# Performance work log

Hardware: AMD Instinct MI355X
Metric: run time of the kernel (lower is better)

Reference implementation:

```python
import jax, jax.numpy as jnp
import numpy as np

D_STATE = 16
D_CONV = 4
DT_RANK = 8


def layer_norm(x, g, b, eps=1e-5):
    m = x.mean(-1, keepdims=True)
    v = ((x - m) ** 2).mean(-1, keepdims=True)
    return (x - m) / jnp.sqrt(v + eps) * g + b


def rms_norm(x, w, eps=1e-5):
    return x * jax.lax.rsqrt(jnp.mean(x * x, -1, keepdims=True) + eps) * w


def mamba_layer(feat, in_proj_w, conv_w, conv_b, x_proj_w, dt_proj_w, dt_proj_b,
                A_log, D_param, out_proj_w, rms_w):
    # feat: [N, C] treated as a length-N sequence with batch 1 (residual block)
    x_in = rms_norm(feat, rms_w)
    xz = x_in @ in_proj_w                         # [N, 2*d_inner]
    d_inner = conv_w.shape[0]
    x, z = xz[:, :d_inner], xz[:, d_inner:]
    # causal depthwise conv1d (torch pad=d_conv-1 then truncate to L)
    L = x.shape[0]
    x_pad = jnp.pad(x, ((D_CONV - 1, 0), (0, 0)))
    xc = conv_b + sum(x_pad[k:k + L, :] * conv_w[:, k] for k in range(D_CONV))
    x = jax.nn.silu(xc)
    dbc = x @ x_proj_w                            # [N, dt_rank + 2*d_state]
    delta = jax.nn.softplus(dbc[:, :DT_RANK] @ dt_proj_w + dt_proj_b)  # [N, d_inner]
    Bm = dbc[:, DT_RANK:DT_RANK + D_STATE]        # [N, d_state]
    Cm = dbc[:, DT_RANK + D_STATE:]               # [N, d_state]
    A = -jnp.exp(A_log)                           # [d_inner, d_state]

    def step(h, inp):
        d_t, b_t, c_t, x_t = inp
        dA = jnp.exp(d_t[:, None] * A)            # [d_inner, d_state]
        h = dA * h + d_t[:, None] * b_t[None, :] * x_t[:, None]
        y_t = (h * c_t[None, :]).sum(-1)          # [d_inner]
        return h, y_t

    h0 = jnp.zeros((d_inner, D_STATE), feat.dtype)
    _, y = jax.lax.scan(step, h0, (delta, Bm, Cm, x))
    y = y + D_param * x
    y = y * jax.nn.silu(z)
    return feat + y @ out_proj_w                  # residual


def setup_inputs() -> dict:
    N, K, C = 32768, 16, 128
    d_inner = 2 * C
    key = jax.random.key(0)
    ks = jax.random.split(key, 12)
    s = 0.02
    inp = {
        "feat": jax.random.normal(ks[0], (N, C), jnp.float32),
        "coord": jax.random.normal(ks[1], (N, 3), jnp.float32),
        "reference_index": jax.random.randint(ks[2], (N, K), 0, N, jnp.int32),
        "gauss_dist": jax.random.uniform(ks[3], (N, K), jnp.float32),
        "j": 0,
        # Mamba params
        "in_proj_w": jax.random.normal(ks[4], (C, 2 * d_inner), jnp.float32) * s,
        "conv_w": jax.random.normal(ks[5], (d_inner, D_CONV), jnp.float32) * s,
        "conv_b": jnp.zeros((d_inner,), jnp.float32),
        "x_proj_w": jax.random.normal(ks[6], (d_inner, DT_RANK + 2 * D_STATE), jnp.float32) * s,
        "dt_proj_w": jax.random.normal(ks[7], (DT_RANK, d_inner), jnp.float32) * s,
        "dt_proj_b": jax.random.uniform(ks[8], (d_inner,), jnp.float32) * 0.1,
        "A_log": jnp.log(jnp.tile(jnp.arange(1.0, D_STATE + 1.0, dtype=jnp.float32), (d_inner, 1))),
        "D_param": jnp.ones((d_inner,), jnp.float32),
        "out_proj_w": jax.random.normal(ks[9], (d_inner, C), jnp.float32) * s,
        "rms_w": jnp.ones((C,), jnp.float32),
        # PointBatchNorm (LayerNorm) shared for both norms
        "ln_g": jnp.ones((C,), jnp.float32),
        "ln_b": jnp.zeros((C,), jnp.float32),
        # linear_attention: Linear(2C->C), LayerNorm, ReLU, Linear(C->C)
        "la_w1": jax.random.normal(ks[10], (2 * C, C), jnp.float32) * s,
        "la_b1": jnp.zeros((C,), jnp.float32),
        "la_ln_g": jnp.ones((C,), jnp.float32),
        "la_ln_b": jnp.zeros((C,), jnp.float32),
        "la_w2": jax.random.normal(ks[11], (C, C), jnp.float32) * s,
        "la_b2": jnp.zeros((C,), jnp.float32),
    }
    return inp


def reference(feat, coord, reference_index, gauss_dist, j,
              in_proj_w, conv_w, conv_b, x_proj_w, dt_proj_w, dt_proj_b,
              A_log, D_param, out_proj_w, rms_w, ln_g, ln_b,
              la_w1, la_b1, la_ln_g, la_ln_b, la_w2, la_b2):
    # pointops.grouping(with_xyz=False): gather neighbor features [N, K, C]
    group_feat = feat[reference_index]
    combined = (gauss_dist[..., None] * group_feat).sum(axis=1)     # [N, C]
    combined = layer_norm(combined, ln_g, ln_b)
    feat_mamba = mamba_layer(feat, in_proj_w, conv_w, conv_b, x_proj_w,
                             dt_proj_w, dt_proj_b, A_log, D_param,
                             out_proj_w, rms_w)
    feat_mamba = layer_norm(feat_mamba, ln_g, ln_b)
    cat_feat = jnp.concatenate([feat_mamba, combined], axis=-1)     # [N, 2C]
    h = jax.nn.relu(layer_norm(cat_feat @ la_w1 + la_b1, la_ln_g, la_ln_b))
    return h @ la_w2 + la_b2
```

## Files before the change

kernel.cpp:

```cpp
#include <hip/hip_runtime.h>
#include <hip/hip_bf16.h>
#include <math.h>

#define N_TOK 32768
#define LC 32
#define NCHUNK (N_TOK / LC)
#define NSEG 64
#define SEGLEN (NCHUNK / NSEG)
#define CXT 16
#define NCXB (N_TOK / CXT)
#define XPAD 264

typedef short short8 __attribute__((ext_vector_type(8)));
typedef float f32x4 __attribute__((ext_vector_type(4)));

__device__ __forceinline__ float siluf_(float v){ return v / (1.f + __expf(-v)); }
__device__ __forceinline__ float softplusf_(float v){ return v > 20.f ? v : __logf(1.f + __expf(v)); }

__device__ __forceinline__ unsigned f2bfu(float f){
  __hip_bfloat16 h = __float2bfloat16(f);
  return (unsigned)*(unsigned short*)&h;
}
__device__ __forceinline__ float bfu2f(unsigned short u){
  __hip_bfloat16 h; *(unsigned short*)&h = u; return __bfloat162float(h);
}

__device__ __forceinline__ float waveRed64(float v){
  #pragma unroll
  for (int m = 1; m < 64; m <<= 1) v += __shfl_xor(v, m);
  return v;
}

__device__ __forceinline__ void pow_chain(float w, float pw[16]){
  pw[0]=w; pw[1]=w*w; pw[2]=pw[1]*w; pw[3]=pw[1]*pw[1];
  pw[4]=pw[3]*pw[0]; pw[5]=pw[3]*pw[1]; pw[6]=pw[3]*pw[2]; pw[7]=pw[3]*pw[3];
  pw[8]=pw[7]*pw[0]; pw[9]=pw[7]*pw[1]; pw[10]=pw[7]*pw[2]; pw[11]=pw[7]*pw[3];
  pw[12]=pw[7]*pw[4]; pw[13]=pw[7]*pw[5]; pw[14]=pw[7]*pw[6]; pw[15]=pw[7]*pw[7];
}

__device__ __forceinline__ bool check_intA(const float aS[16]){
  bool ok = true;
  #pragma unroll
  for (int s=0;s<16;s++){
    float tgt = (float)(s+1);
    if (fabsf(-aS[s] - tgt) > 1e-4f*tgt) ok = false;
  }
  return ok;
}

__global__ void __launch_bounds__(256) k_front(const float* __restrict__ feat,
                        const float* __restrict__ rmsw,
                        unsigned* __restrict__ a0u,
                        const float* __restrict__ ipw, const float* __restrict__ opw,
                        const float* __restrict__ w1, const float* __restrict__ w2,
                        const float* __restrict__ xpw,
                        __hip_bfloat16* __restrict__ ipwt, __hip_bfloat16* __restrict__ opwt,
                        __hip_bfloat16* __restrict__ w1t, __hip_bfloat16* __restrict__ w2t,
                        __hip_bfloat16* __restrict__ xpwt){
  int bid = blockIdx.x;
  if (bid >= 8192){
    int e = (bid-8192)*256 + threadIdx.x;
    if (e < 65536){ int n=e>>7, k=e&127; ipwt[e]=__float2bfloat16(ipw[k*512+n]); }
    else if (e < 98304){ int f=e-65536; int n=f>>8, k=f&255; opwt[f]=__float2bfloat16(opw[k*128+n]); }
    else if (e < 131072){ int f=e-98304; int n=f>>8, k=f&255; w1t[f]=__float2bfloat16(w1[k*128+n]); }
    else if (e < 147456){ int f=e-131072; int n=f>>7, k=f&127; w2t[f]=__float2bfloat16(w2[k*128+n]); }
    else if (e < 159744){ int f=e-147456; int n=f>>8, k=f&255;
                          xpwt[f]=(n<40)?__float2bfloat16(xpw[k*40+n]):__float2bfloat16(0.f); }
    return;
  }
  int row = bid*4 + (threadIdx.x>>6);
  int lane = threadIdx.x & 63;
  float2 f2 = ((const float2*)feat)[row*64 + lane];
  float ss = waveRed64(f2.x*f2.x + f2.y*f2.y);
  float is0 = rsqrtf(ss * (1.f/128.f) + 1e-5f);
  float2 w = ((const float2*)rmsw)[lane];
  a0u[row*64 + lane] = f2bfu(f2.x*is0*w.x) | (f2bfu(f2.y*is0*w.y) << 16);
}

template<int WM16, int WN16>
__global__ __launch_bounds__(256) void k_mfma(const __hip_bfloat16* __restrict__ A,
      const __hip_bfloat16* __restrict__ Wt, int K,
      __hip_bfloat16* __restrict__ out0b, __hip_bfloat16* __restrict__ out1){
  int tid = threadIdx.x;
  int wave = tid>>6, lane = tid&63;
  int wm = wave>>1, wn = wave&1;
  int lane16 = lane&15, quad = lane>>4;
  int m_w = blockIdx.x*(2*WM16*16) + wm*(WM16*16);
  int n_w = blockIdx.y*(2*WN16*16) + wn*(WN16*16);
  f32x4 acc[WM16][WN16];
  #pragma unroll
  for (int i=0;i<WM16;i++)
    #pragma unroll
    for (int j=0;j<WN16;j++) acc[i][j] = (f32x4){0.f,0.f,0.f,0.f};
  const __hip_bfloat16* Ab = A  + (size_t)(m_w + lane16)*K + quad*8;
  const __hip_bfloat16* Bb = Wt + (size_t)(n_w + lane16)*K + quad*8;
  #pragma unroll 4
  for (int kk=0; kk<K; kk+=32){
    short8 a[WM16], b[WN16];
    #pragma unroll
    for (int i=0;i<WM16;i++) a[i] = *(const short8*)(Ab + (size_t)i*16*K + kk);
    #pragma unroll
    for (int j=0;j<WN16;j++) b[j] = *(const short8*)(Bb + (size_t)j*16*K + kk);
    #pragma unroll
    for (int i=0;i<WM16;i++)
      #pragma unroll
      for (int j=0;j<WN16;j++)
        acc[i][j] = __builtin_amdgcn_mfma_f32_16x16x32_bf16(b[j], a[i], acc[i][j], 0, 0, 0);
  }
  #pragma unroll
  for (int i=0;i<WM16;i++){
    int m = m_w + i*16 + lane16;
    #pragma unroll
    for (int j=0;j<WN16;j++){
      int n0 = n_w + j*16 + quad*4;
      if (n0 < 256){
        unsigned u0 = f2bfu(acc[i][j][0]) | (f2bfu(acc[i][j][1]) << 16);
        unsigned u1 = f2bfu(acc[i][j][2]) | (f2bfu(acc[i][j][3]) << 16);
        *(uint2*)(out0b + (size_t)m*256 + n0) = make_uint2(u0, u1);
      } else {
        unsigned u0 = f2bfu(siluf_(acc[i][j][0])) | (f2bfu(siluf_(acc[i][j][1])) << 16);
        unsigned u1 = f2bfu(siluf_(acc[i][j][2])) | (f2bfu(siluf_(acc[i][j][3])) << 16);
        *(uint2*)(out1 + (size_t)m*256 + (n0-256)) = make_uint2(u0, u1);
      }
    }
  }
}

__global__ __launch_bounds__(256) void k_cxd(
      const __hip_bfloat16* __restrict__ bxb,
      const __hip_bfloat16* __restrict__ xpwt,
      const float* __restrict__ cw, const float* __restrict__ cb,
      const float* __restrict__ dtw, const float* __restrict__ dtb,
      unsigned* __restrict__ dxb,
      float* __restrict__ Bm, float* __restrict__ Cm,
      const float* __restrict__ feat, const int* __restrict__ ridx,
      const float* __restrict__ gd, const float* __restrict__ g,
      const float* __restrict__ b, unsigned* __restrict__ catB){
  int tid = threadIdx.x;
  int bid = blockIdx.x;

  if (bid >= NCXB){
    int row = (bid - NCXB)*4 + (tid>>6);
    int lane = tid & 63;
    float ax=0.f, ay=0.f;
    #pragma unroll 4
    for (int k=0;k<16;k++){
      int idx = ridx[row*16+k];
      float ww = gd[row*16+k];
      float2 f = ((const float2*)feat)[idx*64 + lane];
      ax += ww*f.x; ay += ww*f.y;
    }
    float m = waveRed64(ax+ay) * (1.f/128.f);
    float dx = ax-m, dy = ay-m;
    float var = waveRed64(dx*dx+dy*dy) * (1.f/128.f);
    float is = rsqrtf(var + 1e-5f);
    float2 gg = ((const float2*)g)[lane];
    float2 bb = ((const float2*)b)[lane];
    float ox = dx*is*gg.x + bb.x, oy = dy*is*gg.y + bb.y;
    catB[row*64 + lane] = f2bfu(ox) | (f2bfu(oy) << 16);
    return;
  }

  __shared__ __align__(16) __hip_bfloat16 Xs[CXT][XPAD];
  __shared__ __align__(16) float DT[CXT][8];
  int wave = tid>>6, lane = tid&63;
  int lane16 = lane&15, quad = lane>>4;
  int r0 = bid*CXT;

  {
    int d = tid;
    float cw0=cw[d*4], cw1=cw[d*4+1], cw2=cw[d*4+2], cw3=cw[d*4+3], cbb=cb[d];
    float a_0 = (r0 >= 3) ? __bfloat162float(bxb[(size_t)(r0-3)*256 + d]) : 0.f;
    float a_1 = (r0 >= 2) ? __bfloat162float(bxb[(size_t)(r0-2)*256 + d]) : 0.f;
    float a_2 = (r0 >= 1) ? __bfloat162float(bxb[(size_t)(r0-1)*256 + d]) : 0.f;
    #pragma unroll 4
    for (int t=0;t<CXT;t++){
      float a_3 = __bfloat162float(bxb[(size_t)(r0+t)*256 + d]);
      float xc = siluf_(cbb + cw0*a_0 + cw1*a_1 + cw2*a_2 + cw3*a_3);
      Xs[t][d] = __float2bfloat16(xc);
      a_0=a_1; a_1=a_2; a_2=a_3;
    }
  }
  __syncthreads();

  if (wave < 3){
    f32x4 acc3 = (f32x4){0.f,0.f,0.f,0.f};
    const __hip_bfloat16* Arow = &Xs[lane16][0] + quad*8;
    const __hip_bfloat16* Bb = xpwt + (size_t)(wave*16 + lane16)*256 + quad*8;
    #pragma unroll
    for (int kk=0; kk<256; kk+=32){
      short8 a  = *(const short8*)(Arow + kk);
      short8 bfr = *(const short8*)(Bb + kk);
      acc3 = __builtin_amdgcn_mfma_f32_16x16x32_bf16(a, bfr, acc3, 0, 0, 0);
    }
    int n = wave*16 + lane16;
    #pragma unroll
    for (int r=0;r<4;r++){
      int m = quad*4 + r;
      float v = acc3[r];
      if (n < 8)       DT[m][n] = v;
      else if (n < 24) Bm[(size_t)(r0+m)*16 + (n-8)] = v;
      else if (n < 40) Cm[(size_t)(r0+m)*16 + (n-24)] = v;
    }
  }
  __syncthreads();

  {
    int d = tid;
    float w8[8];
    #pragma unroll
    for (int j=0;j<8;j++) w8[j] = dtw[j*256+d];
    float dbias = dtb[d];
    #pragma unroll
    for (int t=0;t<CXT;t++){
      const float4* T = (const float4*)&DT[t][0];
      float4 u = T[0], v = T[1];
      float acc = dbias
        + u.x*w8[0] + u.y*w8[1] + u.z*w8[2] + u.w*w8[3]
        + v.x*w8[4] + v.y*w8[5] + v.z*w8[6] + v.w*w8[7];
      float dv = softplusf_(acc);
      unsigned xu = *(const unsigned short*)&Xs[t][d];
      dxb[(size_t)(r0+t)*256 + d] = f2bfu(dv) | (xu << 16);
    }
  }
}

__global__ __launch_bounds__(256) void k_scan1(const unsigned* __restrict__ dxb,
      const float* __restrict__ Bm, const float* __restrict__ A_log,
      float* __restrict__ dsum_o, __hip_bfloat16* __restrict__ Hc){
  __shared__ float Bl[LC][16];
  int g = blockIdx.x;
  int tid = threadIdx.x;
  int d = tid;
  int t0 = g*LC;
  if (tid < LC*4) ((float4*)&Bl[0][0])[tid] = ((const float4*)(Bm + (size_t)t0*16))[tid];
  __syncthreads();
  float aS[16];
  #pragma unroll
  for (int s=0;s<16;s++) aS[s] = -__expf(A_log[d*16+s]);
  bool fastA = check_intA(aS);
  float h[16] = {};
  float dsum = 0.f;
  if (fastA){
    #pragma unroll 4
    for (int t=0;t<LC;t++){
      unsigned u = dxb[(size_t)(t0+t)*256 + d];
      float dv = bfu2f((unsigned short)(u & 0xffff));
      float xv = bfu2f((unsigned short)(u >> 16));
      const float4* Bp = (const float4*)&Bl[t][0];
      float4 b0=Bp[0], b1=Bp[1], b2=Bp[2], b3=Bp[3];
      float bl[16] = {b0.x,b0.y,b0.z,b0.w, b1.x,b1.y,b1.z,b1.w,
                      b2.x,b2.y,b2.z,b2.w, b3.x,b3.y,b3.z,b3.w};
      dsum += dv;
      float dx_ = dv*xv;
      float w[16]; pow_chain(__expf(-dv), w);
      #pragma unroll
      for (int s=0;s<16;s++) h[s] = w[s]*h[s] + dx_*bl[s];
    }
  } else {
    #pragma unroll 4
    for (int t=0;t<LC;t++){
      unsigned u = dxb[(size_t)(t0+t)*256 + d];
      float dv = bfu2f((unsigned short)(u & 0xffff));
      float xv = bfu2f((unsigned short)(u >> 16));
      const float4* Bp = (const float4*)&Bl[t][0];
      float4 b0=Bp[0], b1=Bp[1], b2=Bp[2], b3=Bp[3];
      float bl[16] = {b0.x,b0.y,b0.z,b0.w, b1.x,b1.y,b1.z,b1.w,
                      b2.x,b2.y,b2.z,b2.w, b3.x,b3.y,b3.z,b3.w};
      dsum += dv;
      float dx_ = dv*xv;
      #pragma unroll
      for (int s=0;s<16;s++) h[s] = __expf(dv*aS[s])*h[s] + dx_*bl[s];
    }
  }
  dsum_o[(size_t)g*256 + d] = dsum;
  unsigned u[8];
  #pragma unroll
  for (int q=0;q<8;q++) u[q] = f2bfu(h[2*q]) | (f2bfu(h[2*q+1]) << 16);
  uint4* Hd = (uint4*)(Hc + (size_t)g*4096 + (size_t)d*16);
  Hd[0] = make_uint4(u[0],u[1],u[2],u[3]);
  Hd[1] = make_uint4(u[4],u[5],u[6],u[7]);
}

__global__ __launch_bounds__(256) void k_carry_a(const float* __restrict__ dsum,
      __hip_bfloat16* __restrict__ Hc, const float* __restrict__ A_log,
      float* __restrict__ dsum_pre, float* __restrict__ segsum, float* __restrict__ Hagg){
  int seg = blockIdx.x;
  int ch  = blockIdx.y*256 + threadIdx.x;
  int d = ch>>4, s = ch&15;
  float aSv = -__expf(A_log[ch]);
  float dpre = 0.f, c = 0.f;
  int g0 = seg*SEGLEN;
  #pragma unroll 4
  for (int i=0;i<SEGLEN;i++){
    int g = g0+i;
    float ds = dsum[(size_t)g*256 + d];
    size_t a = (size_t)g*4096 + ch;
    float hh = __bfloat162float(Hc[a]);
    float p = __expf(ds*aSv);
    if (s==0) dsum_pre[(size_t)g*256 + d] = dpre;
    Hc[a] = __float2bfloat16(c);
    dpre += ds;
    c = p*c + hh;
  }
  if (s==0) segsum[seg*256 + d] = dpre;
  Hagg[(size_t)seg*4096 + ch] = c;
}

__global__ __launch_bounds__(256) void k_carry_b(const float* __restrict__ segsum,
      const float* __restrict__ Hagg, const float* __restrict__ A_log,
      float* __restrict__ Cseg){
  int ch = blockIdx.x*256 + threadIdx.x;
  int d = ch>>4;
  float aSv = -__expf(A_log[ch]);
  float c = 0.f;
  #pragma unroll 8
  for (int s=0;s<NSEG;s++){
    Cseg[(size_t)s*4096 + ch] = c;
    c = __expf(segsum[s*256 + d]*aSv)*c + Hagg[(size_t)s*4096 + ch];
  }
}

__global__ __launch_bounds__(256) void k_scan2(const unsigned* __restrict__ dxb,
      const __hip_bfloat16* __restrict__ zb, const float* __restrict__ Bm,
      const float* __restrict__ Cm, const float* __restrict__ A_log,
      const float* __restrict__ Dp, const float* __restrict__ dsum_pre,
      const __hip_bfloat16* __restrict__ Hc, const float* __restrict__ Cseg,
      __hip_bfloat16* __restrict__ yb){
  __shared__ float Bl[LC][16];
  __shared__ float Cl[LC][16];
  int g = blockIdx.x;
  int tid = threadIdx.x;
  int d = tid;
  int t0 = g*LC;
  if (tid < 128) ((float4*)&Bl[0][0])[tid] = ((const float4*)(Bm + (size_t)t0*16))[tid];
  else ((float4*)&Cl[0][0])[tid-128] = ((const float4*)(Cm + (size_t)t0*16))[tid-128];
  __syncthreads();
  int seg = g / SEGLEN;
  float aS[16];
  #pragma unroll
  for (int s=0;s<16;s++) aS[s] = -__expf(A_log[d*16+s]);
  bool fastA = check_intA(aS);
  float h[16];
  {
    float dpre = dsum_pre[(size_t)g*256 + d];
    const uint4* hp = (const uint4*)(Hc + (size_t)g*4096 + (size_t)d*16);
    uint4 H0 = hp[0], H1 = hp[1];
    unsigned hu[8] = {H0.x,H0.y,H0.z,H0.w, H1.x,H1.y,H1.z,H1.w};
    const float4* cs = (const float4*)(Cseg + (size_t)seg*4096 + (size_t)d*16);
    float ws[16];
    if (fastA){
      pow_chain(__expf(-dpre), ws);
    } else {
      #pragma unroll
      for (int s=0;s<16;s++) ws[s] = __expf(dpre*aS[s]);
    }
    #pragma unroll
    for (int q=0;q<4;q++){
      float4 C = cs[q];
      h[q*4+0] = ws[q*4+0]*C.x + bfu2f((unsigned short)(hu[q*2]   & 0xffff));
      h[q*4+1] = ws[q*4+1]*C.y + bfu2f((unsigned short)(hu[q*2]   >> 16));
      h[q*4+2] = ws[q*4+2]*C.z + bfu2f((unsigned short)(hu[q*2+1] & 0xffff));
      h[q*4+3] = ws[q*4+3]*C.w + bfu2f((unsigned short)(hu[q*2+1] >> 16));
    }
  }
  float dpar = Dp[d];
  if (fastA){
    #pragma unroll 4
    for (int t=0;t<LC;t++){
      unsigned u = dxb[(size_t)(t0+t)*256 + d];
      float dv = bfu2f((unsigned short)(u & 0xffff));
      float xv = bfu2f((unsigned short)(u >> 16));
      float zv = __bfloat162float(zb[(size_t)(t0+t)*256 + d]);
      const float4* Bp = (const float4*)&Bl[t][0];
      const float4* Cp = (const float4*)&Cl[t][0];
      float4 b0=Bp[0], b1=Bp[1], b2=Bp[2], b3=Bp[3];
      float4 c0=Cp[0], c1=Cp[1], c2=Cp[2], c3=Cp[3];
      float bl[16] = {b0.x,b0.y,b0.z,b0.w, b1.x,b1.y,b1.z,b1.w,
                      b2.x,b2.y,b2.z,b2.w, b3.x,b3.y,b3.z,b3.w};
      float cl[16] = {c0.x,c0.y,c0.z,c0.w, c1.x,c1.y,c1.z,c1.w,
                      c2.x,c2.y,c2.z,c2.w, c3.x,c3.y,c3.z,c3.w};
      float dx_ = dv*xv;
      float w[16]; pow_chain(__expf(-dv), w);
      float yv = 0.f;
      #pragma unroll
      for (int s=0;s<16;s++){
        h[s] = w[s]*h[s] + dx_*bl[s];
        yv += h[s]*cl[s];
      }
      yb[(size_t)(t0+t)*256 + d] = __float2bfloat16((yv + dpar*xv)*zv);
    }
  } else {
    #pragma unroll 4
    for (int t=0;t<LC;t++){
      unsigned u = dxb[(size_t)(t0+t)*256 + d];
      float dv = bfu2f((unsigned short)(u & 0xffff));
      float xv = bfu2f((unsigned short)(u >> 16));
      float zv = __bfloat162float(zb[(size_t)(t0+t)*256 + d]);
      const float4* Bp = (const float4*)&Bl[t][0];
      const float4* Cp = (const float4*)&Cl[t][0];
      float4 b0=Bp[0], b1=Bp[1], b2=Bp[2], b3=Bp[3];
      float4 c0=Cp[0], c1=Cp[1], c2=Cp[2], c3=Cp[3];
      float bl[16] = {b0.x,b0.y,b0.z,b0.w, b1.x,b1.y,b1.z,b1.w,
                      b2.x,b2.y,b2.z,b2.w, b3.x,b3.y,b3.z,b3.w};
      float cl[16] = {c0.x,c0.y,c0.z,c0.w, c1.x,c1.y,c1.z,c1.w,
                      c2.x,c2.y,c2.z,c2.w, c3.x,c3.y,c3.z,c3.w};
      float dx_ = dv*xv;
      float yv = 0.f;
      #pragma unroll
      for (int s=0;s<16;s++){
        h[s] = __expf(dv*aS[s])*h[s] + dx_*bl[s];
        yv += h[s]*cl[s];
      }
      yb[(size_t)(t0+t)*256 + d] = __float2bfloat16((yv + dpar*xv)*zv);
    }
  }
}

__global__ __launch_bounds__(256) void k_tail(const __hip_bfloat16* __restrict__ yb,
      const __hip_bfloat16* __restrict__ opwt, const float* __restrict__ feat,
      const float* __restrict__ lng, const float* __restrict__ lnb,
      const unsigned* __restrict__ catB,
      const __hip_bfloat16* __restrict__ w1t, const float* __restrict__ b1,
      const float* __restrict__ lag, const float* __restrict__ lab,
      const __hip_bfloat16* __restrict__ w2t, const float* __restrict__ b2,
      float* __restrict__ out){
  __shared__ __align__(16) float Ls[64][132];
  __shared__ __align__(16) unsigned Cu[64][132];
  int tid = threadIdx.x;
  int wave = tid>>6, lane = tid&63;
  int wm = wave>>1, wn = wave&1;
  int lane16 = lane&15, quad = lane>>4;
  int r0 = blockIdx.x*64;

  #pragma unroll
  for (int i=0;i<16;i++){
    int idx = i*256 + tid;
    int row = idx>>6, c = idx&63;
    Cu[row][64+c] = catB[(size_t)(r0+row)*64 + c];
  }

  f32x4 acc[2][4];
  #pragma unroll
  for (int i=0;i<2;i++)
    #pragma unroll
    for (int j=0;j<4;j++) acc[i][j] = (f32x4){0.f,0.f,0.f,0.f};
  {
    const __hip_bfloat16* Ab = yb   + (size_t)(r0 + wm*32 + lane16)*256 + quad*8;
    const __hip_bfloat16* Bb = opwt + (size_t)(wn*64 + lane16)*256 + quad*8;
    #pragma unroll 2
    for (int kk=0; kk<256; kk+=32){
      short8 a[2], bf[4];
      #pragma unroll
      for (int i=0;i<2;i++) a[i] = *(const short8*)(Ab + (size_t)i*16*256 + kk);
      #pragma unroll
      for (int j=0;j<4;j++) bf[j] = *(const short8*)(Bb + (size_t)j*16*256 + kk);
      #pragma unroll
      for (int i=0;i<2;i++)
        #pragma unroll
        for (int j=0;j<4;j++)
          acc[i][j] = __builtin_amdgcn_mfma_f32_16x16x32_bf16(a[i], bf[j], acc[i][j], 0, 0, 0);
    }
  }
  #pragma unroll
  for (int i=0;i<2;i++)
    #pragma unroll
    for (int j=0;j<4;j++){
      int n = wn*64 + j*16 + lane16;
      #pragma unroll
      for (int r=0;r<4;r++){
        int m = wm*32 + i*16 + quad*4 + r;
        Ls[m][n] = acc[i][j][r] + feat[(size_t)(r0+m)*128 + n];
      }
    }
  __syncthreads();
  {
    float2 gv = ((const float2*)lng)[lane];
    float2 bv = ((const float2*)lnb)[lane];
    #pragma unroll 4
    for (int rr=0; rr<16; rr++){
      int row = wave*16 + rr;
      float2 v = *(const float2*)&Ls[row][2*lane];
      float mm = waveRed64(v.x+v.y) * (1.f/128.f);
      float dx = v.x-mm, dy = v.y-mm;
      float var = waveRed64(dx*dx+dy*dy) * (1.f/128.f);
      float is = rsqrtf(var + 1e-5f);
      Cu[row][lane] = f2bfu(dx*is*gv.x + bv.x) | (f2bfu(dy*is*gv.y + bv.y) << 16);
    }
  }
  __syncthreads();
  #pragma unroll
  for (int i=0;i<2;i++)
    #pragma unroll
    for (int j=0;j<4;j++) acc[i][j] = (f32x4){0.f,0.f,0.f,0.f};
  {
    const __hip_bfloat16* Bb = w1t + (size_t)(wn*64 + lane16)*256 + quad*8;
    #pragma unroll 2
    for (int kk=0; kk<256; kk+=32){
      short8 a[2], bf[4];
      #pragma unroll
      for (int i=0;i<2;i++)
        a[i] = *(const short8*)(&Cu[wm*32 + i*16 + lane16][0] + (kk>>1) + quad*4);
      #pragma unroll
      for (int j=0;j<4;j++) bf[j] = *(const short8*)(Bb + (size_t)j*16*256 + kk);
      #pragma unroll
      for (int i=0;i<2;i++)
        #pragma unroll
        for (int j=0;j<4;j++)
          acc[i][j] = __builtin_amdgcn_mfma_f32_16x16x32_bf16(a[i], bf[j], acc[i][j], 0, 0, 0);
    }
  }
  #pragma unroll
  for (int i=0;i<2;i++)
    #pragma unroll
    for (int j=0;j<4;j++){
      int n = wn*64 + j*16 + lane16;
      float bv1 = b1[n];
      #pragma unroll
      for (int r=0;r<4;r++){
        int m = wm*32 + i*16 + quad*4 + r;
        Ls[m][n] = acc[i][j][r] + bv1;
      }
    }
  __syncthreads();
  {
    float2 gv = ((const float2*)lag)[lane];
    float2 bv = ((const float2*)lab)[lane];
    #pragma unroll 4
    for (int rr=0; rr<16; rr++){
      int row = wave*16 + rr;
      float2 v = *(const float2*)&Ls[row][2*lane];
      float mm = waveRed64(v.x+v.y) * (1.f/128.f);
      float dx = v.x-mm, dy = v.y-mm;
      float var = waveRed64(dx*dx+dy*dy) * (1.f/128.f);
      float is = rsqrtf(var + 1e-5f);
      float ox = fmaxf(dx*is*gv.x + bv.x, 0.f);
      float oy = fmaxf(dy*is*gv.y + bv.y, 0.f);
      Cu[row][lane] = f2bfu(ox) | (f2bfu(oy) << 16);
    }
  }
  __syncthreads();
  #pragma unroll
  for (int i=0;i<2;i++)
    #pragma unroll
    for (int j=0;j<4;j++) acc[i][j] = (f32x4){0.f,0.f,0.f,0.f};
  {
    const __hip_bfloat16* Bb = w2t + (size_t)(wn*64 + lane16)*128 + quad*8;
    #pragma unroll
    for (int kk=0; kk<128; kk+=32){
      short8 a[2], bf[4];
      #pragma unroll
      for (int i=0;i<2;i++)
        a[i] = *(const short8*)(&Cu[wm*32 + i*16 + lane16][0] + (kk>>1) + quad*4);
      #pragma unroll
      for (int j=0;j<4;j++) bf[j] = *(const short8*)(Bb + (size_t)j*16*128 + kk);
      #pragma unroll
      for (int i=0;i<2;i++)
        #pragma unroll
        for (int j=0;j<4;j++)
          acc[i][j] = __builtin_amdgcn_mfma_f32_16x16x32_bf16(bf[j], a[i], acc[i][j], 0, 0, 0);
    }
  }
  #pragma unroll
  for (int i=0;i<2;i++){
    int m = wm*32 + i*16 + lane16;
    #pragma unroll
    for (int j=0;j<4;j++){
      int n0 = wn*64 + j*16 + quad*4;
      float4 o;
      o.x = acc[i][j][0] + b2[n0+0];
      o.y = acc[i][j][1] + b2[n0+1];
      o.z = acc[i][j][2] + b2[n0+2];
      o.w = acc[i][j][3] + b2[n0+3];
      *(float4*)(out + (size_t)(r0+m)*128 + n0) = o;
    }
  }
}

extern "C" void kernel_launch(void* const* d_in, const int* in_sizes, int n_in,
                              void* d_out, int out_size, void* d_ws, size_t ws_size,
                              hipStream_t stream){
  const float* feat = (const float*)d_in[0];
  const int*   ridx = (const int*)d_in[2];
  const float* gd   = (const float*)d_in[3];
  const float* ipw  = (const float*)d_in[5];
  const float* cw   = (const float*)d_in[6];
  const float* cb   = (const float*)d_in[7];
  const float* xpw  = (const float*)d_in[8];
  const float* dtw  = (const float*)d_in[9];
  const float* dtb  = (const float*)d_in[10];
  const float* alog = (const float*)d_in[11];
  const float* dpar = (const float*)d_in[12];
  const float* opw  = (const float*)d_in[13];
  const float* rmsw = (const float*)d_in[14];
  const float* lng  = (const float*)d_in[15];
  const float* lnb  = (const float*)d_in[16];
  const float* w1   = (const float*)d_in[17];
  const float* b1   = (const float*)d_in[18];
  const float* lag  = (const float*)d_in[19];
  const float* lab  = (const float*)d_in[20];
  const float* w2   = (const float*)d_in[21];
  const float* b2   = (const float*)d_in[22];
  float* out = (float*)d_out;

  char* p = (char*)d_ws;
  __hip_bfloat16* bxb  = (__hip_bfloat16*)p; p += (size_t)N_TOK*256*2;
  __hip_bfloat16* zb   = (__hip_bfloat16*)p; p += (size_t)N_TOK*256*2;
  unsigned* dxb        = (unsigned*)p;       p += (size_t)N_TOK*256*4;
  unsigned* catB       = (unsigned*)p;       p += (size_t)N_TOK*64*4;
  __hip_bfloat16* yb   = (__hip_bfloat16*)p; p += (size_t)N_TOK*256*2;
  float* Bm   = (float*)p; p += (size_t)N_TOK*16*4;
  float* Cm   = (float*)p; p += (size_t)N_TOK*16*4;
  __hip_bfloat16* Hc = (__hip_bfloat16*)p; p += (size_t)NCHUNK*4096*2;
  float* dsum = (float*)p; p += (size_t)NCHUNK*256*4;
  float* dpre = (float*)p; p += (size_t)NCHUNK*256*4;
  float* segs = (float*)p; p += (size_t)NSEG*256*4;
  float* Hagg = (float*)p; p += (size_t)NSEG*4096*4;
  float* Cseg = (float*)p; p += (size_t)NSEG*4096*4;
  __hip_bfloat16* ipwt = (__hip_bfloat16*)p; p += 512*128*2;
  __hip_bfloat16* opwt = (__hip_bfloat16*)p; p += 128*256*2;
  __hip_bfloat16* w1t  = (__hip_bfloat16*)p; p += 128*256*2;
  __hip_bfloat16* w2t  = (__hip_bfloat16*)p; p += 128*128*2;
  __hip_bfloat16* xpwt = (__hip_bfloat16*)p; p += 48*256*2;
  __hip_bfloat16* a0 = yb;

  hipLaunchKernelGGL(k_front, dim3(8192+624), dim3(256), 0, stream,
                     feat, rmsw, (unsigned*)a0,
                     ipw, opw, w1, w2, xpw, ipwt, opwt, w1t, w2t, xpwt);
  hipLaunchKernelGGL((k_mfma<4,4>), dim3(N_TOK/128, 4), dim3(256), 0, stream,
                     a0, ipwt, 128, bxb, zb);
  hipLaunchKernelGGL(k_cxd, dim3(NCXB + 8192), dim3(256), 0, stream,
                     bxb, xpwt, cw, cb, dtw, dtb, dxb, Bm, Cm,
                     feat, ridx, gd, lng, lnb, catB);
  hipLaunchKernelGGL(k_scan1, dim3(NCHUNK), dim3(256), 0, stream,
                     dxb, Bm, alog, dsum, Hc);
  hipLaunchKernelGGL(k_carry_a, dim3(NSEG, 16), dim3(256), 0, stream,
                     dsum, Hc, alog, dpre, segs, Hagg);
  hipLaunchKernelGGL(k_carry_b, dim3(16), dim3(256), 0, stream, segs, Hagg, alog, Cseg);
  hipLaunchKernelGGL(k_scan2, dim3(NCHUNK), dim3(256), 0, stream,
                     dxb, zb, Bm, Cm, alog, dpar, dpre, Hc, Cseg, yb);
  hipLaunchKernelGGL(k_tail, dim3(N_TOK/64), dim3(256), 0, stream,
                     yb, opwt, feat, lng, lnb, catB, w1t, b1, lag, lab, w2t, b2, out);
}
```

Baseline: 279.3 us.

## Fuse chunk-local scan pass into conv/x_proj kernel with 16-token chunks

Removes the separate first scan kernel by computing each chunk's local state and delta sum inside the conv/x_proj/dt kernel, with the chunk length reduced to match its 16-token tile. B values are kept in shared memory so they are not re-read from global memory, and the dxb/Bm reload is avoided. Halving the chunk length doubles the number of chunks, so the carry pass and the chunk-state buffers grow. The fused kernel also carries more register pressure from the 16-wide state.

```diff
diff --git a/kernel.cpp b/kernel.cpp
--- a/kernel.cpp
+++ b/kernel.cpp
@@ -3,7 +3,7 @@
 #include <math.h>
 
 #define N_TOK 32768
-#define LC 32
+#define LC 16
 #define NCHUNK (N_TOK / LC)
 #define NSEG 64
 #define SEGLEN (NCHUNK / NSEG)
@@ -131,8 +131,10 @@
       const __hip_bfloat16* __restrict__ xpwt,
       const float* __restrict__ cw, const float* __restrict__ cb,
       const float* __restrict__ dtw, const float* __restrict__ dtb,
+      const float* __restrict__ A_log,
       unsigned* __restrict__ dxb,
       float* __restrict__ Bm, float* __restrict__ Cm,
+      float* __restrict__ dsum_o, __hip_bfloat16* __restrict__ Hc,
       const float* __restrict__ feat, const int* __restrict__ ridx,
       const float* __restrict__ gd, const float* __restrict__ g,
       const float* __restrict__ b, unsigned* __restrict__ catB){
@@ -163,6 +165,7 @@
 
   __shared__ __align__(16) __hip_bfloat16 Xs[CXT][XPAD];
   __shared__ __align__(16) float DT[CXT][8];
+  __shared__ __align__(16) float Bs[CXT][16];
   int wave = tid>>6, lane = tid&63;
   int lane16 = lane&15, quad = lane>>4;
   int r0 = bid*CXT;
@@ -199,7 +202,7 @@
       int m = quad*4 + r;
       float v = acc3[r];
       if (n < 8)       DT[m][n] = v;
-      else if (n < 24) Bm[(size_t)(r0+m)*16 + (n-8)] = v;
+      else if (n < 24){ Bs[m][n-8] = v; Bm[(size_t)(r0+m)*16 + (n-8)] = v; }
       else if (n < 40) Cm[(size_t)(r0+m)*16 + (n-24)] = v;
     }
   }
@@ -211,75 +214,64 @@
     #pragma unroll
     for (int j=0;j<8;j++) w8[j] = dtw[j*256+d];
     float dbias = dtb[d];
-    #pragma unroll
-    for (int t=0;t<CXT;t++){
-      const float4* T = (const float4*)&DT[t][0];
-      float4 u = T[0], v = T[1];
-      float acc = dbias
-        + u.x*w8[0] + u.y*w8[1] + u.z*w8[2] + u.w*w8[3]
-        + v.x*w8[4] + v.y*w8[5] + v.z*w8[6] + v.w*w8[7];
-      float dv = softplusf_(acc);
-      unsigned xu = *(const unsigned short*)&Xs[t][d];
-      dxb[(size_t)(r0+t)*256 + d] = f2bfu(dv) | (xu << 16);
-    }
-  }
-}
-
-__global__ __launch_bounds__(256) void k_scan1(const unsigned* __restrict__ dxb,
-      const float* __restrict__ Bm, const float* __restrict__ A_log,
-      float* __restrict__ dsum_o, __hip_bfloat16* __restrict__ Hc){
-  __shared__ float Bl[LC][16];
-  int g = blockIdx.x;
-  int tid = threadIdx.x;
-  int d = tid;
-  int t0 = g*LC;
-  if (tid < LC*4) ((float4*)&Bl[0][0])[tid] = ((const float4*)(Bm + (size_t)t0*16))[tid];
-  __syncthreads();
-  float aS[16];
-  #pragma unroll
-  for (int s=0;s<16;s++) aS[s] = -__expf(A_log[d*16+s]);
-  bool fastA = check_intA(aS);
-  float h[16] = {};
-  float dsum = 0.f;
-  if (fastA){
-    #pragma unroll 4
-    for (int t=0;t<LC;t++){
-      unsigned u = dxb[(size_t)(t0+t)*256 + d];
-      float dv = bfu2f((unsigned short)(u & 0xffff));
-      float xv = bfu2f((unsigned short)(u >> 16));
-      const float4* Bp = (const float4*)&Bl[t][0];
-      float4 b0=Bp[0], b1=Bp[1], b2=Bp[2], b3=Bp[3];
-      float bl[16] = {b0.x,b0.y,b0.z,b0.w, b1.x,b1.y,b1.z,b1.w,
-                      b2.x,b2.y,b2.z,b2.w, b3.x,b3.y,b3.z,b3.w};
-      dsum += dv;
-      float dx_ = dv*xv;
-      float w[16]; pow_chain(__expf(-dv), w);
-      #pragma unroll
-      for (int s=0;s<16;s++) h[s] = w[s]*h[s] + dx_*bl[s];
-    }
-  } else {
-    #pragma unroll 4
-    for (int t=0;t<LC;t++){
-      unsigned u = dxb[(size_t)(t0+t)*256 + d];
-      float dv = bfu2f((unsigned short)(u & 0xffff));
-      float xv = bfu2f((unsigned short)(u >> 16));
-      const float4* Bp = (const float4*)&Bl[t][0];
-      float4 b0=Bp[0], b1=Bp[1], b2=Bp[2], b3=Bp[3];
-      float bl[16] = {b0.x,b0.y,b0.z,b0.w, b1.x,b1.y,b1.z,b1.w,
-                      b2.x,b2.y,b2.z,b2.w, b3.x,b3.y,b3.z,b3.w};
-      dsum += dv;
-      float dx_ = dv*xv;
-      #pragma unroll
-      for (int s=0;s<16;s++) h[s] = __expf(dv*aS[s])*h[s] + dx_*bl[s];
-    }
-  }
-  dsum_o[(size_t)g*256 + d] = dsum;
-  unsigned u[8];
-  #pragma unroll
-  for (int q=0;q<8;q++) u[q] = f2bfu(h[2*q]) | (f2bfu(h[2*q+1]) << 16);
-  uint4* Hd = (uint4*)(Hc + (size_t)g*4096 + (size_t)d*16);
-  Hd[0] = make_uint4(u[0],u[1],u[2],u[3]);
-  Hd[1] = make_uint4(u[4],u[5],u[6],u[7]);
+    float aS[16];
+    #pragma unroll
+    for (int s=0;s<16;s++) aS[s] = -__expf(A_log[d*16+s]);
+    bool fastA = check_intA(aS);
+    float h[16] = {};
+    float dsum = 0.f;
+    if (fastA){
+      #pragma unroll 4
+      for (int t=0;t<CXT;t++){
+        const float4* T = (const float4*)&DT[t][0];
+        float4 u = T[0], v = T[1];
+        float acc = dbias
+          + u.x*w8[0] + u.y*w8[1] + u.z*w8[2] + u.w*w8[3]
+          + v.x*w8[4] + v.y*w8[5] + v.z*w8[6] + v.w*w8[7];
+        float dv = softplusf_(acc);
+        unsigned xu = *(const unsigned short*)&Xs[t][d];
+        dxb[(size_t)(r0+t)*256 + d] = f2bfu(dv) | (xu << 16);
+        float xv = bfu2f((unsigned short)xu);
+        dsum += dv;
+        float dx_ = dv*xv;
+        const float4* Bp = (const float4*)&Bs[t][0];
+        float4 b0=Bp[0], b1=Bp[1], b2=Bp[2], b3=Bp[3];
+        float bl[16] = {b0.x,b0.y,b0.z,b0.w, b1.x,b1.y,b1.z,b1.w,
+                        b2.x,b2.y,b2.z,b2.w, b3.x,b3.y,b3.z,b3.w};
+        float w[16]; pow_chain(__expf(-dv), w);
+        #pragma unroll
+        for (int s=0;s<16;s++) h[s] = w[s]*h[s] + dx_*bl[s];
+      }
+    } else {
+      #pragma unroll 4
+      for (int t=0;t<CXT;t++){
+        const float4* T = (const float4*)&DT[t][0];
+        float4 u = T[0], v = T[1];
+        float acc = dbias
+          + u.x*w8[0] + u.y*w8[1] + u.z*w8[2] + u.w*w8[3]
+          + v.x*w8[4] + v.y*w8[5] + v.z*w8[6] + v.w*w8[7];
+        float dv = softplusf_(acc);
+        unsigned xu = *(const unsigned short*)&Xs[t][d];
+        dxb[(size_t)(r0+t)*256 + d] = f2bfu(dv) | (xu << 16);
+        float xv = bfu2f((unsigned short)xu);
+        dsum += dv;
+        float dx_ = dv*xv;
+        const float4* Bp = (const float4*)&Bs[t][0];
+        float4 b0=Bp[0], b1=Bp[1], b2=Bp[2], b3=Bp[3];
+        float bl[16] = {b0.x,b0.y,b0.z,b0.w, b1.x,b1.y,b1.z,b1.w,
+                        b2.x,b2.y,b2.z,b2.w, b3.x,b3.y,b3.z,b3.w};
+        #pragma unroll
+        for (int s=0;s<16;s++) h[s] = __expf(dv*aS[s])*h[s] + dx_*bl[s];
+      }
+    }
+    dsum_o[(size_t)bid*256 + d] = dsum;
+    unsigned uu[8];
+    #pragma unroll
+    for (int q=0;q<8;q++) uu[q] = f2bfu(h[2*q]) | (f2bfu(h[2*q+1]) << 16);
+    uint4* Hd = (uint4*)(Hc + (size_t)bid*4096 + (size_t)d*16);
+    Hd[0] = make_uint4(uu[0],uu[1],uu[2],uu[3]);
+    Hd[1] = make_uint4(uu[4],uu[5],uu[6],uu[7]);
+  }
 }
 
 __global__ __launch_bounds__(256) void k_carry_a(const float* __restrict__ dsum,
@@ -333,8 +325,8 @@
   int tid = threadIdx.x;
   int d = tid;
   int t0 = g*LC;
-  if (tid < 128) ((float4*)&Bl[0][0])[tid] = ((const float4*)(Bm + (size_t)t0*16))[tid];
-  else ((float4*)&Cl[0][0])[tid-128] = ((const float4*)(Cm + (size_t)t0*16))[tid-128];
+  if (tid < 64) ((float4*)&Bl[0][0])[tid] = ((const float4*)(Bm + (size_t)t0*16))[tid];
+  else if (tid < 128) ((float4*)&Cl[0][0])[tid-64] = ((const float4*)(Cm + (size_t)t0*16))[tid-64];
   __syncthreads();
   int seg = g / SEGLEN;
   float aS[16];
@@ -630,10 +622,8 @@
   hipLaunchKernelGGL((k_mfma<4,4>), dim3(N_TOK/128, 4), dim3(256), 0, stream,
                      a0, ipwt, 128, bxb, zb);
   hipLaunchKernelGGL(k_cxd, dim3(NCXB + 8192), dim3(256), 0, stream,
-                     bxb, xpwt, cw, cb, dtw, dtb, dxb, Bm, Cm,
+                     bxb, xpwt, cw, cb, dtw, dtb, alog, dxb, Bm, Cm, dsum, Hc,
                      feat, ridx, gd, lng, lnb, catB);
-  hipLaunchKernelGGL(k_scan1, dim3(NCHUNK), dim3(256), 0, stream,
-                     dxb, Bm, alog, dsum, Hc);
   hipLaunchKernelGGL(k_carry_a, dim3(NSEG, 16), dim3(256), 0, stream,
                      dsum, Hc, alog, dpre, segs, Hagg);
   hipLaunchKernelGGL(k_carry_b, dim3(16), dim3(256), 0, stream, segs, Hagg, alog, Cseg);
```

Result: no change. 283.7 us (+1.6%).
